# Optimization experiments

Hardware: AMD Instinct MI355X
Metric: run time of the kernel (lower is better)

## Reference

```python
import jax, jax.numpy as jnp
import numpy as np

B, D, H = 64, 512, 512          # batch c, spatial dim D, feature dim H == channel
CIN = 4 * H                     # concat of 4 branches
HID = CIN // 4                  # reduction=4


def _gcn_norm_adj():
    # fixed 4-node fully-connected graph, GCNConv default: add self loops,
    # symmetric normalization D^{-1/2} (A+I) D^{-1/2}
    ei = np.array([[0, 1, 0, 2, 0, 3, 1, 2, 1, 3, 2, 3],
                   [1, 0, 2, 0, 3, 0, 2, 1, 3, 1, 3, 2]])
    A = np.zeros((4, 4), np.float32)
    A[ei[1], ei[0]] = 1.0               # message src -> dst
    A += np.eye(4, dtype=np.float32)    # self loops
    dinv = 1.0 / np.sqrt(A.sum(1))
    return jnp.asarray(dinv[:, None] * A * dinv[None, :])  # (4,4)


def setup_inputs() -> dict:
    key = jax.random.key(0)
    ks = jax.random.split(key, 32)

    def rn(k, shape, s=0.02):
        return jax.random.normal(k, shape, dtype=jnp.float32) * s

    inp = {}
    for i in range(4):
        inp[f"fea{i+1}"] = jax.random.normal(ks[i], (B, D, H), dtype=jnp.float32)
    inp["W_gcn"] = rn(ks[4], (H, H))
    inp["b_gcn"] = jnp.zeros((H,), jnp.float32)
    for i in range(4):
        inp[f"W1_{i+1}"] = rn(ks[5 + 4 * i], (CIN, HID))
        inp[f"b1_{i+1}"] = jnp.zeros((HID,), jnp.float32)
        inp[f"W2_{i+1}"] = rn(ks[6 + 4 * i], (HID, H))
        inp[f"b2_{i+1}"] = jnp.zeros((H,), jnp.float32)
    return inp


def reference(fea1, fea2, fea3, fea4, W_gcn, b_gcn,
              W1_1, b1_1, W2_1, b2_1,
              W1_2, b1_2, W2_2, b2_2,
              W1_3, b1_3, W2_3, b2_3,
              W1_4, b1_4, W2_4, b2_4):
    A = _gcn_norm_adj()                                   # (4,4)
    y = jnp.stack((fea1, fea2, fea3, fea4), axis=1)       # (B,4,D,H)
    # GCNConv batched over all samples: Ahat_norm @ (X W) + b
    xw = jnp.einsum('bndh,hk->bndk', y, W_gcn)            # (B,4,D,H)
    yg = jnp.einsum('mn,bndk->bmdk', A, xw) + b_gcn       # (B,4,D,H)
    z = jnp.concatenate([yg[:, 0], yg[:, 1], yg[:, 2], yg[:, 3]], axis=2)  # (B,D,4H)

    def gate(W1, b1, W2, b2, fea):
        h = jax.nn.relu(z @ W1 + b1)                      # (B,D,HID)
        g = jax.nn.sigmoid(h @ W2 + b2)                   # (B,D,H)
        return jax.nn.relu(g) * fea

    return (gate(W1_1, b1_1, W2_1, b2_1, fea1),
            gate(W1_2, b1_2, W2_2, b2_2, fea2),
            gate(W1_3, b1_3, W2_3, b2_3, fea3),
            gate(W1_4, b1_4, W2_4, b2_4, fea4))
```

## Files before the change

### kernel.cpp

```cpp
#include <hip/hip_runtime.h>
#include <math.h>

#define MM 32768
#define KK 512
#define NN 512
#define BM 128
#define BN 128
#define BK 32
#define NT (KK / BK)

typedef float  f32x4  __attribute__((ext_vector_type(4)));
typedef __bf16 bf16x8 __attribute__((ext_vector_type(8)));
typedef unsigned short u16x8 __attribute__((ext_vector_type(8)));
typedef unsigned short u16x4 __attribute__((ext_vector_type(4)));

__device__ __forceinline__ unsigned short f2bf(float f) {
    union { float f; unsigned int u; } v; v.f = f;
    unsigned int r = v.u + 0x7fffu + ((v.u >> 16) & 1u);
    return (unsigned short)(r >> 16);
}

__device__ __forceinline__ float bf2f(unsigned short h) {
    union { unsigned int u; float f; } v; v.u = ((unsigned int)h) << 16;
    return v.f;
}

__device__ __forceinline__ void gl_lds16(const void* g, void* l) {
    __builtin_amdgcn_global_load_lds((const __attribute__((address_space(1))) void*)g,
                                     (__attribute__((address_space(3))) void*)l,
                                     16, 0, 0);
}

__global__ __launch_bounds__(256)
void fsum_cast(const float* __restrict__ f1, const float* __restrict__ f2,
               const float* __restrict__ f3, const float* __restrict__ f4,
               unsigned short* __restrict__ out)
{
    const long i = ((long)blockIdx.x * 256 + threadIdx.x) * 8;
    f32x4 s0 = *(const f32x4*)(f1 + i);
    f32x4 s1 = *(const f32x4*)(f1 + i + 4);
    s0 += *(const f32x4*)(f2 + i);  s1 += *(const f32x4*)(f2 + i + 4);
    s0 += *(const f32x4*)(f3 + i);  s1 += *(const f32x4*)(f3 + i + 4);
    s0 += *(const f32x4*)(f4 + i);  s1 += *(const f32x4*)(f4 + i + 4);
    u16x8 o;
    o[0] = f2bf(s0[0]); o[1] = f2bf(s0[1]); o[2] = f2bf(s0[2]); o[3] = f2bf(s0[3]);
    o[4] = f2bf(s1[0]); o[5] = f2bf(s1[1]); o[6] = f2bf(s1[2]); o[7] = f2bf(s1[3]);
    *(u16x8*)(out + i) = o;
}

struct WArgs {
    const float* src[9];
    unsigned short* dst[9];
};

__global__ __launch_bounds__(256)
void wprep(WArgs a)
{
    __shared__ float t[32][33];
    const int z  = blockIdx.z;
    const float* __restrict__ src = a.src[z];
    unsigned short* __restrict__ dst = a.dst[z];
    const int k0 = blockIdx.x * 32;
    const int n0 = blockIdx.y * 32;
    const int tx = threadIdx.x;
    if (z == 0) {
        for (int kk = threadIdx.y; kk < 32; kk += 8) {
            float v = src[(long)(k0 + kk) * 512 + n0 + tx];
            dst[(long)(k0 + kk) * 512 + n0 + tx] = f2bf(0.25f * v);
        }
        return;
    }
    for (int kk = threadIdx.y; kk < 32; kk += 8) {
        float v = src[(long)(k0 + kk) * 512 + n0 + tx];
        if (z >= 1 && z <= 4) {
            v += src[(long)(512  + k0 + kk) * 512 + n0 + tx];
            v += src[(long)(1024 + k0 + kk) * 512 + n0 + tx];
            v += src[(long)(1536 + k0 + kk) * 512 + n0 + tx];
        }
        t[kk][tx] = v;
    }
    __syncthreads();
    for (int nn = threadIdx.y; nn < 32; nn += 8) {
        dst[(long)(n0 + nn) * 512 + k0 + tx] = f2bf(t[tx][nn]);
    }
}

struct BArgs {
    const unsigned short* w1t[4];
    const float* b1[4];
    float* out[4];
};

__global__ __launch_bounds__(256)
void bprep(const float* __restrict__ bg, BArgs a)
{
    __shared__ float bgs[512];
    const int z = blockIdx.x;
    const int tid = threadIdx.x;
    bgs[tid]       = bg[tid];
    bgs[tid + 256] = bg[tid + 256];
    __syncthreads();
    const unsigned short* __restrict__ w = a.w1t[z];
    for (int n = tid; n < 512; n += 256) {
        float acc = 0.0f;
        const unsigned short* row = w + (long)n * 512;
        #pragma unroll 4
        for (int t = 0; t < 512; t += 8) {
            u16x8 wv = *(const u16x8*)(row + t);
            #pragma unroll
            for (int jj = 0; jj < 8; ++jj) acc += bgs[t + jj] * bf2f(wv[jj]);
        }
        a.out[z][n] = acc + a.b1[z][n];
    }
}

struct GArgs {
    const unsigned short* A[4];
    const unsigned short* Bt[4];
    const float* bias[4];
    const float* fea[4];
    void* out[4];
};

__device__ __forceinline__ void stage4(const unsigned short* gb, unsigned short* lb, int r) {
    #pragma unroll
    for (int c = 0; c < 4; ++c)
        gl_lds16(gb + (long)(c * 16 + r) * KK, lb + c * 16 * BK);
}

template<int MODE>
__global__ __launch_bounds__(256)
void gemm_ep(GArgs a)
{
    __shared__ __attribute__((aligned(16))) unsigned short As[3][BM * BK];
    __shared__ __attribute__((aligned(16))) unsigned short Bs[3][BN * BK];

    const int z = blockIdx.z;
    const unsigned short* __restrict__ A  = a.A[z];
    const unsigned short* __restrict__ Bt = a.Bt[z];
    const float* __restrict__ bias = a.bias[z];
    const float* __restrict__ fea  = a.fea[z];
    void* __restrict__ out = a.out[z];

    const int tid  = threadIdx.x;
    const int lane = tid & 63;
    const int wave = tid >> 6;
    const int m0 = blockIdx.x * BM;
    const int n0 = blockIdx.y * BN;

    const bool isA = (wave < 2);
    const int rowbase = (wave & 1) * 64;
    const unsigned short* gsrc = isA ? A : Bt;
    const int r   = lane >> 2;
    const int cb  = lane & 3;
    const int cbs = cb ^ ((r >> 1) & 3);
    const long grow0 = (isA ? (long)m0 : (long)n0) + rowbase;
    const unsigned short* gbase0 = gsrc + grow0 * KK + cbs * 8;
    unsigned short* lb[3] = {
        (isA ? As[0] : Bs[0]) + rowbase * BK,
        (isA ? As[1] : Bs[1]) + rowbase * BK,
        (isA ? As[2] : Bs[2]) + rowbase * BK };

    const int frow = lane & 15;
    const int fk   = ((lane >> 4) ^ ((frow >> 1) & 3)) * 8;
    const int wrow = wave >> 1;
    const int wcol = wave & 1;

    f32x4 acc[4][4] = {};

    stage4(gbase0 + 0 * BK, lb[0], r);
    stage4(gbase0 + 1 * BK, lb[1], r);
    stage4(gbase0 + 2 * BK, lb[2], r);

    #pragma unroll
    for (int ks = 0; ks < NT; ++ks) {
        if      (ks < NT - 2) asm volatile("s_waitcnt vmcnt(8)" ::: "memory");
        else if (ks == NT - 2) asm volatile("s_waitcnt vmcnt(4)" ::: "memory");
        else                   asm volatile("s_waitcnt vmcnt(0)" ::: "memory");
        __builtin_amdgcn_s_barrier();
        asm volatile("" ::: "memory");

        const unsigned short* Asc = As[ks % 3];
        const unsigned short* Bsc = Bs[ks % 3];
        bf16x8 afr[4], bfr[4];
        #pragma unroll
        for (int i = 0; i < 4; ++i)
            afr[i] = *(const bf16x8*)(Asc + (wrow * 64 + i * 16 + frow) * BK + fk);
        #pragma unroll
        for (int j = 0; j < 4; ++j)
            bfr[j] = *(const bf16x8*)(Bsc + (wcol * 64 + j * 16 + frow) * BK + fk);

        #pragma unroll
        for (int i = 0; i < 4; ++i)
            #pragma unroll
            for (int j = 0; j < 4; ++j)
                acc[i][j] = __builtin_amdgcn_mfma_f32_16x16x32_bf16(
                    bfr[j], afr[i], acc[i][j], 0, 0, 0);

        asm volatile("" ::: "memory");
        __builtin_amdgcn_s_barrier();
        asm volatile("" ::: "memory");
        if (ks + 3 < NT)
            stage4(gbase0 + (ks + 3) * BK, lb[ks % 3], r);
    }

    const int mr  = lane & 15;
    const int cq4 = (lane >> 4) * 4;
    #pragma unroll
    for (int j = 0; j < 4; ++j) {
        const int col = n0 + wcol * 64 + j * 16 + cq4;
        f32x4 bv;
        if (MODE == 3) { bv[0] = bv[1] = bv[2] = bv[3] = 0.0f; }
        else           { bv = *(const f32x4*)(bias + col); }
        #pragma unroll
        for (int i = 0; i < 4; ++i) {
            const long row = m0 + wrow * 64 + i * 16 + mr;
            f32x4 v = acc[i][j] + bv;
            if (MODE == 1) {
                u16x4 o;
                o[0] = f2bf(fmaxf(v[0], 0.0f)); o[1] = f2bf(fmaxf(v[1], 0.0f));
                o[2] = f2bf(fmaxf(v[2], 0.0f)); o[3] = f2bf(fmaxf(v[3], 0.0f));
                *(u16x4*)((unsigned short*)out + row * NN + col) = o;
            } else if (MODE == 3) {
                u16x4 o;
                o[0] = f2bf(v[0]); o[1] = f2bf(v[1]);
                o[2] = f2bf(v[2]); o[3] = f2bf(v[3]);
                *(u16x4*)((unsigned short*)out + row * NN + col) = o;
            } else {
                f32x4 fv = *(const f32x4*)(fea + row * NN + col);
                f32x4 o;
                #pragma unroll
                for (int q = 0; q < 4; ++q) {
                    float e = __expf(-v[q]);
                    o[q] = __fdividef(fv[q], 1.0f + e);
                }
                *(f32x4*)((float*)out + row * NN + col) = o;
            }
        }
    }
}

extern "C" void kernel_launch(void* const* d_in, const int* in_sizes, int n_in,
                              void* d_out, int out_size, void* d_ws, size_t ws_size,
                              hipStream_t stream)
{
    (void)in_sizes; (void)n_in; (void)out_size; (void)ws_size;

    const float* fea[4] = {(const float*)d_in[0], (const float*)d_in[1],
                           (const float*)d_in[2], (const float*)d_in[3]};
    const float* W_gcn = (const float*)d_in[4];
    const float* b_gcn = (const float*)d_in[5];
    const float *W1[4], *b1[4], *W2[4], *b2[4];
    for (int i = 0; i < 4; ++i) {
        W1[i] = (const float*)d_in[6 + 4 * i];
        b1[i] = (const float*)d_in[7 + 4 * i];
        W2[i] = (const float*)d_in[8 + 4 * i];
        b2[i] = (const float*)d_in[9 + 4 * i];
    }

    const size_t MB = 1024 * 1024;
    char* ws = (char*)d_ws;
    unsigned short* fsum_h = (unsigned short*)ws;
    unsigned short* wbuf   = (unsigned short*)(ws + 32 * MB);
    unsigned short* Wgb = wbuf;
    unsigned short *W1T[4], *W2T[4], *WcT[4], *hbuf[4];
    for (int i = 0; i < 4; ++i) {
        W1T[i] = wbuf + (size_t)(1 + i) * 262144;
        W2T[i] = wbuf + (size_t)(5 + i) * 262144;
        WcT[i] = (unsigned short*)(ws + 40 * MB) + (size_t)i * 262144;
        hbuf[i] = (unsigned short*)(ws + 48 * MB + (size_t)i * 32 * MB);
    }
    float* bcomb = (float*)(ws + 44 * MB);

    fsum_cast<<<8192, 256, 0, stream>>>(fea[0], fea[1], fea[2], fea[3], fsum_h);

    WArgs wa;
    wa.src[0] = W_gcn; wa.dst[0] = Wgb;
    for (int i = 0; i < 4; ++i) { wa.src[1 + i] = W1[i]; wa.dst[1 + i] = W1T[i]; }
    for (int i = 0; i < 4; ++i) { wa.src[5 + i] = W2[i]; wa.dst[5 + i] = W2T[i]; }
    wprep<<<dim3(16, 16, 9), dim3(32, 8), 0, stream>>>(wa);

    BArgs ba;
    for (int i = 0; i < 4; ++i) { ba.w1t[i] = W1T[i]; ba.b1[i] = b1[i]; ba.out[i] = bcomb + (size_t)i * 512; }
    bprep<<<4, 256, 0, stream>>>(b_gcn, ba);

    GArgs g3;
    for (int i = 0; i < 4; ++i) {
        g3.A[i] = W1T[i]; g3.Bt[i] = Wgb; g3.bias[i] = nullptr;
        g3.fea[i] = nullptr; g3.out[i] = WcT[i];
    }
    gemm_ep<3><<<dim3(4, 4, 4), 256, 0, stream>>>(g3);

    GArgs g1;
    for (int i = 0; i < 4; ++i) {
        g1.A[i] = fsum_h; g1.Bt[i] = WcT[i]; g1.bias[i] = bcomb + (size_t)i * 512;
        g1.fea[i] = nullptr; g1.out[i] = hbuf[i];
    }
    gemm_ep<1><<<dim3(MM / BM, NN / BN, 4), 256, 0, stream>>>(g1);

    float* outp = (float*)d_out;
    GArgs g2;
    for (int i = 0; i < 4; ++i) {
        g2.A[i] = hbuf[i]; g2.Bt[i] = W2T[i]; g2.bias[i] = b2[i];
        g2.fea[i] = fea[i]; g2.out[i] = outp + (size_t)i * MM * NN;
    }
    gemm_ep<2><<<dim3(MM / BM, NN / BN, 4), 256, 0, stream>>>(g2);
}
```

Measured before the change: 828.9 us.

## Fuse the two MLP GEMMs into one kernel keeping hidden activations in LDS

Replaces the two separate GEMM launches (z·W1 with ReLU, then h·W2 with sigmoid gate) with a single fused kernel. Each workgroup computes a 128-row slice of the hidden activations in 128-column chunks, writes them to swizzled LDS as bf16, and immediately accumulates the second GEMM. This removes the round trip of the 128 MB hidden buffer through global memory. In exchange, the fused kernel reads A and B fragments straight from global memory without LDS staging or prefetch, and it holds a large accumulator array that may limit occupancy.

Measured after the change: 1.085 ms. 1.31x slower.

```diff
diff --git a/kernel.cpp b/kernel.cpp
--- a/kernel.cpp
+++ b/kernel.cpp
@@ -138,8 +138,6 @@
     const int z = blockIdx.z;
     const unsigned short* __restrict__ A  = a.A[z];
     const unsigned short* __restrict__ Bt = a.Bt[z];
-    const float* __restrict__ bias = a.bias[z];
-    const float* __restrict__ fea  = a.fea[z];
     void* __restrict__ out = a.out[z];
 
     const int tid  = threadIdx.x;
@@ -174,7 +172,7 @@
 
     #pragma unroll
     for (int ks = 0; ks < NT; ++ks) {
-        if      (ks < NT - 2) asm volatile("s_waitcnt vmcnt(8)" ::: "memory");
+        if      (ks < NT - 2)  asm volatile("s_waitcnt vmcnt(8)" ::: "memory");
         else if (ks == NT - 2) asm volatile("s_waitcnt vmcnt(4)" ::: "memory");
         else                   asm volatile("s_waitcnt vmcnt(0)" ::: "memory");
         __builtin_amdgcn_s_barrier();
@@ -209,33 +207,138 @@
     #pragma unroll
     for (int j = 0; j < 4; ++j) {
         const int col = n0 + wcol * 64 + j * 16 + cq4;
-        f32x4 bv;
-        if (MODE == 3) { bv[0] = bv[1] = bv[2] = bv[3] = 0.0f; }
-        else           { bv = *(const f32x4*)(bias + col); }
         #pragma unroll
         for (int i = 0; i < 4; ++i) {
             const long row = m0 + wrow * 64 + i * 16 + mr;
-            f32x4 v = acc[i][j] + bv;
-            if (MODE == 1) {
+            f32x4 v = acc[i][j];
+            u16x4 o;
+            o[0] = f2bf(v[0]); o[1] = f2bf(v[1]);
+            o[2] = f2bf(v[2]); o[3] = f2bf(v[3]);
+            *(u16x4*)((unsigned short*)out + row * NN + col) = o;
+        }
+    }
+}
+
+struct FArgs {
+    const unsigned short* WcT[4];
+    const unsigned short* W2T[4];
+    const float* bcomb[4];
+    const float* b2[4];
+    const float* fea[4];
+    float* out[4];
+    const unsigned short* fsum;
+};
+
+__global__ __launch_bounds__(512, 2)
+void fused_mlp(FArgs a)
+{
+    __shared__ __attribute__((aligned(16))) unsigned short hlds[128 * 128];
+
+    const int wg  = blockIdx.x;
+    const int gt  = (wg & 7) * 128 + (wg >> 3);
+    const int z   = gt & 3;
+    const int m0  = (gt >> 2) * 128;
+
+    const int tid  = threadIdx.x;
+    const int lane = tid & 63;
+    const int wave = tid >> 6;
+    const int wm = wave >> 2;
+    const int wn = wave & 3;
+    const int fr = lane & 15;
+    const int fq = lane >> 4;
+
+    const unsigned short* __restrict__ Afs = a.fsum;
+    const unsigned short* __restrict__ Wc  = a.WcT[z];
+    const unsigned short* __restrict__ W2  = a.W2T[z];
+    const float* __restrict__ bc  = a.bcomb[z];
+    const float* __restrict__ b2  = a.b2[z];
+    const float* __restrict__ fea = a.fea[z];
+    float* __restrict__ out = a.out[z];
+
+    f32x4 acc2[4][8] = {};
+
+    for (int c = 0; c < 4; ++c) {
+        f32x4 acc1[4][2] = {};
+        #pragma unroll 4
+        for (int ks = 0; ks < 16; ++ks) {
+            bf16x8 afr[4], bfr[2];
+            #pragma unroll
+            for (int mi = 0; mi < 4; ++mi)
+                afr[mi] = *(const bf16x8*)(Afs +
+                    (long)(m0 + wm * 64 + mi * 16 + fr) * 512 + ks * 32 + fq * 8);
+            #pragma unroll
+            for (int ni = 0; ni < 2; ++ni)
+                bfr[ni] = *(const bf16x8*)(Wc +
+                    (long)(c * 128 + wn * 32 + ni * 16 + fr) * 512 + ks * 32 + fq * 8);
+            #pragma unroll
+            for (int mi = 0; mi < 4; ++mi)
+                #pragma unroll
+                for (int ni = 0; ni < 2; ++ni)
+                    acc1[mi][ni] = __builtin_amdgcn_mfma_f32_16x16x32_bf16(
+                        bfr[ni], afr[mi], acc1[mi][ni], 0, 0, 0);
+        }
+
+        asm volatile("" ::: "memory");
+        __builtin_amdgcn_s_barrier();
+        asm volatile("" ::: "memory");
+
+        #pragma unroll
+        for (int mi = 0; mi < 4; ++mi) {
+            #pragma unroll
+            for (int ni = 0; ni < 2; ++ni) {
+                const int colh = wn * 32 + ni * 16 + fq * 4;
+                const f32x4 bcv = *(const f32x4*)(bc + c * 128 + colh);
+                const int row = wm * 64 + mi * 16 + fr;
                 u16x4 o;
-                o[0] = f2bf(fmaxf(v[0], 0.0f)); o[1] = f2bf(fmaxf(v[1], 0.0f));
-                o[2] = f2bf(fmaxf(v[2], 0.0f)); o[3] = f2bf(fmaxf(v[3], 0.0f));
-                *(u16x4*)((unsigned short*)out + row * NN + col) = o;
-            } else if (MODE == 3) {
-                u16x4 o;
-                o[0] = f2bf(v[0]); o[1] = f2bf(v[1]);
-                o[2] = f2bf(v[2]); o[3] = f2bf(v[3]);
-                *(u16x4*)((unsigned short*)out + row * NN + col) = o;
-            } else {
-                f32x4 fv = *(const f32x4*)(fea + row * NN + col);
-                f32x4 o;
                 #pragma unroll
-                for (int q = 0; q < 4; ++q) {
-                    float e = __expf(-v[q]);
-                    o[q] = __fdividef(fv[q], 1.0f + e);
-                }
-                *(f32x4*)((float*)out + row * NN + col) = o;
+                for (int q = 0; q < 4; ++q)
+                    o[q] = f2bf(fmaxf(acc1[mi][ni][q] + bcv[q], 0.0f));
+                const int byte = row * 256 + ((colh * 2) ^ ((row & 7) << 4));
+                *(u16x4*)((char*)hlds + byte) = o;
             }
+        }
+        asm volatile("s_waitcnt lgkmcnt(0)" ::: "memory");
+        __builtin_amdgcn_s_barrier();
+        asm volatile("" ::: "memory");
+
+        #pragma unroll
+        for (int ks2 = 0; ks2 < 4; ++ks2) {
+            bf16x8 hfr[4], b2fr[8];
+            #pragma unroll
+            for (int mi = 0; mi < 4; ++mi) {
+                const int row = wm * 64 + mi * 16 + fr;
+                const int byte = row * 256 + ((ks2 * 64 + fq * 16) ^ ((row & 7) << 4));
+                hfr[mi] = *(const bf16x8*)((const char*)hlds + byte);
+            }
+            #pragma unroll
+            for (int ni = 0; ni < 8; ++ni)
+                b2fr[ni] = *(const bf16x8*)(W2 +
+                    (long)(wn * 128 + ni * 16 + fr) * 512 + c * 128 + ks2 * 32 + fq * 8);
+            #pragma unroll
+            for (int mi = 0; mi < 4; ++mi)
+                #pragma unroll
+                for (int ni = 0; ni < 8; ++ni)
+                    acc2[mi][ni] = __builtin_amdgcn_mfma_f32_16x16x32_bf16(
+                        b2fr[ni], hfr[mi], acc2[mi][ni], 0, 0, 0);
+        }
+    }
+
+    #pragma unroll
+    for (int ni = 0; ni < 8; ++ni) {
+        const int col = wn * 128 + ni * 16 + fq * 4;
+        const f32x4 bv = *(const f32x4*)(b2 + col);
+        #pragma unroll
+        for (int mi = 0; mi < 4; ++mi) {
+            const long row = m0 + wm * 64 + mi * 16 + fr;
+            f32x4 v = acc2[mi][ni] + bv;
+            f32x4 fv = *(const f32x4*)(fea + row * 512 + col);
+            f32x4 o;
+            #pragma unroll
+            for (int q = 0; q < 4; ++q) {
+                const float e = __expf(-v[q]);
+                o[q] = __fdividef(fv[q], 1.0f + e);
+            }
+            *(f32x4*)(out + row * 512 + col) = o;
         }
     }
 }
@@ -263,12 +366,11 @@
     unsigned short* fsum_h = (unsigned short*)ws;
     unsigned short* wbuf   = (unsigned short*)(ws + 32 * MB);
     unsigned short* Wgb = wbuf;
-    unsigned short *W1T[4], *W2T[4], *WcT[4], *hbuf[4];
+    unsigned short *W1T[4], *W2T[4], *WcT[4];
     for (int i = 0; i < 4; ++i) {
         W1T[i] = wbuf + (size_t)(1 + i) * 262144;
         W2T[i] = wbuf + (size_t)(5 + i) * 262144;
         WcT[i] = (unsigned short*)(ws + 40 * MB) + (size_t)i * 262144;
-        hbuf[i] = (unsigned short*)(ws + 48 * MB + (size_t)i * 32 * MB);
     }
     float* bcomb = (float*)(ws + 44 * MB);
 
@@ -291,18 +393,12 @@
     }
     gemm_ep<3><<<dim3(4, 4, 4), 256, 0, stream>>>(g3);
 
-    GArgs g1;
+    FArgs fa;
     for (int i = 0; i < 4; ++i) {
-        g1.A[i] = fsum_h; g1.Bt[i] = WcT[i]; g1.bias[i] = bcomb + (size_t)i * 512;
-        g1.fea[i] = nullptr; g1.out[i] = hbuf[i];
-    }
-    gemm_ep<1><<<dim3(MM / BM, NN / BN, 4), 256, 0, stream>>>(g1);
-
-    float* outp = (float*)d_out;
-    GArgs g2;
-    for (int i = 0; i < 4; ++i) {
-        g2.A[i] = hbuf[i]; g2.Bt[i] = W2T[i]; g2.bias[i] = b2[i];
-        g2.fea[i] = fea[i]; g2.out[i] = outp + (size_t)i * MM * NN;
-    }
-    gemm_ep<2><<<dim3(MM / BM, NN / BN, 4), 256, 0, stream>>>(g2);
-}
+        fa.WcT[i] = WcT[i]; fa.W2T[i] = W2T[i];
+        fa.bcomb[i] = bcomb + (size_t)i * 512; fa.b2[i] = b2[i];
+        fa.fea[i] = fea[i]; fa.out[i] = (float*)d_out + (size_t)i * MM * NN;
+    }
+    fa.fsum = fsum_h;
+    fused_mlp<<<1024, 512, 0, stream>>>(fa);
+}
```
